# Kernel tuning notes

Hardware: AMD Instinct MI355X
Metric: run time of the kernel (lower is better)

The kernel has to match this reference:

```python
import jax, jax.numpy as jnp
import numpy as np
from jax import lax

WS = 8      # window size (square)
SS = 4      # shift size
HEADS = 8
K = 9       # snake-conv kernel size
CENTER = K // 2
EXT = 1.0   # extend_scope


def _shift_attn_mask(H, W):
    # static numpy construction of Swin shift mask -> [num_windows, L, L]
    m = np.zeros((H, W), dtype=np.float32)
    cnt = 0
    for hs in [(0, -WS), (-WS, -SS), (-SS, None)]:
        for ws_ in [(0, -WS), (-WS, -SS), (-SS, None)]:
            m[hs[0]:hs[1], ws_[0]:ws_[1]] = cnt
            cnt += 1
    m = m.reshape(H // WS, WS, W // WS, WS).transpose(0, 2, 1, 3).reshape(-1, WS * WS)
    d = m[:, None, :] - m[:, :, None]
    return jnp.asarray(np.where(d != 0, -100.0, 0.0).astype(np.float32))


def shifted_window_attention(x, qkv_w, qkv_b, proj_w, proj_b, rel_bias):
    B, H, W, C = x.shape
    d = C // HEADS
    x = jnp.roll(x, shift=(-SS, -SS), axis=(1, 2))
    nH, nW = H // WS, W // WS
    nwin, L = nH * nW, WS * WS
    # window partition -> [B*nwin, L, C]
    xw = x.reshape(B, nH, WS, nW, WS, C).transpose(0, 1, 3, 2, 4, 5).reshape(B * nwin, L, C)
    qkv = (xw @ qkv_w.T + qkv_b).reshape(B * nwin, L, 3, HEADS, d).transpose(2, 0, 3, 1, 4)
    q, k, v = qkv[0] * (d ** -0.5), qkv[1], qkv[2]
    attn = jnp.einsum('nhld,nhmd->nhlm', q, k) + rel_bias[None]
    amask = _shift_attn_mask(H, W)  # [nwin, L, L]
    attn = attn.reshape(B, nwin, HEADS, L, L) + amask[None, :, None]
    attn = jax.nn.softmax(attn.reshape(B * nwin, HEADS, L, L), axis=-1)
    out = jnp.einsum('nhlm,nhmd->nhld', attn, v).transpose(0, 2, 1, 3).reshape(B * nwin, L, C)
    out = out @ proj_w.T + proj_b
    out = out.reshape(B, nH, nW, WS, WS, C).transpose(0, 1, 3, 2, 4, 5).reshape(B, H, W, C)
    return jnp.roll(out, shift=(SS, SS), axis=(1, 2))


def snake_coordinate_map(offset):
    # offset [B, 2K, Wd, Hd], morph=0: cumulative y offsets from the kernel center
    B, _, Wd, Hd = offset.shape
    y_off = offset[:, :K]
    # y_new[center]=0; y_new[center+i]=sum_{j=1..i} y_off[center+j]; mirror below
    up = jnp.cumsum(y_off[:, CENTER + 1:], axis=1)
    down = jnp.cumsum(y_off[:, :CENTER][:, ::-1], axis=1)[:, ::-1]
    y_cum = jnp.concatenate([down, jnp.zeros((B, 1, Wd, Hd), offset.dtype), up], axis=1)
    y_center = jnp.arange(Wd, dtype=offset.dtype)[None, None, :, None]
    y_new = y_center + EXT * y_cum                              # [B,K,Wd,Hd]
    x_spread = jnp.linspace(-CENTER, CENTER, K, dtype=offset.dtype)[None, :, None, None]
    x_center = jnp.arange(Hd, dtype=offset.dtype)[None, None, None, :]
    x_new = jnp.broadcast_to(x_center + x_spread, (B, K, Wd, Hd))
    # rearrange 'b k w h -> b (w k) h'
    y_map = y_new.transpose(0, 2, 1, 3).reshape(B, Wd * K, Hd)
    x_map = x_new.transpose(0, 2, 1, 3).reshape(B, Wd * K, Hd)
    return y_map, x_map


def bilinear_sample(feat, ymap, xmap):
    Hin, Win = feat.shape[-2], feat.shape[-1]
    y = jnp.clip(ymap, 0.0, Hin - 1.0)
    x = jnp.clip(xmap, 0.0, Win - 1.0)
    y0f, x0f = jnp.floor(y), jnp.floor(x)
    wy, wx = y - y0f, x - x0f
    y0 = y0f.astype(jnp.int32); x0 = x0f.astype(jnp.int32)
    y1 = jnp.minimum(y0 + 1, Hin - 1); x1 = jnp.minimum(x0 + 1, Win - 1)
    g = jax.vmap(lambda f, yy, xx: f[:, yy, xx])  # -> [B,C,Ho,Wo]
    v00 = g(feat, y0, x0); v01 = g(feat, y0, x1)
    v10 = g(feat, y1, x0); v11 = g(feat, y1, x1)
    wy = wy[:, None]; wx = wx[:, None]
    return v00 * (1 - wy) * (1 - wx) + v01 * (1 - wy) * wx + v10 * wy * (1 - wx) + v11 * wy * wx


def _forward(x, qkv_weight, qkv_bias, proj_weight, proj_bias, rel_bias, offset, dsc_weight, dsc_bias):
    y = shifted_window_attention(x, qkv_weight, qkv_bias, proj_weight, proj_bias, rel_bias)
    feat = y.transpose(0, 3, 1, 2)                      # NCHW
    ymap, xmap = snake_coordinate_map(offset)
    samp = bilinear_sample(feat, ymap, xmap)            # [B,C,H*K,W]
    out = lax.conv_general_dilated(samp, dsc_weight, window_strides=(K, 1), padding='VALID',
                                   dimension_numbers=('NCHW', 'OIHW', 'NCHW'))
    return jax.nn.relu(out + dsc_bias[None, :, None, None])


def setup_inputs() -> dict:
    key = jax.random.key(0)
    ks = jax.random.split(key, 9)
    B, H, W, C = 8, 64, 64, 256
    return {
        'x': jax.random.normal(ks[0], (B, H, W, C), jnp.float32),
        'qkv_weight': jax.random.normal(ks[1], (3 * C, C), jnp.float32) * 0.05,
        'qkv_bias': jax.random.normal(ks[2], (3 * C,), jnp.float32) * 0.05,
        'proj_weight': jax.random.normal(ks[3], (C, C), jnp.float32) * 0.05,
        'proj_bias': jax.random.normal(ks[4], (C,), jnp.float32) * 0.05,
        'rel_bias': jax.random.normal(ks[5], (HEADS, WS * WS, WS * WS), jnp.float32) * 0.05,
        'offset': jax.random.normal(ks[6], (B, 2 * K, H, W), jnp.float32),
        'dsc_weight': jax.random.normal(ks[7], (C, C, K, 1), jnp.float32) * 0.02,
        'dsc_bias': jax.random.normal(ks[8], (C,), jnp.float32) * 0.02,
    }


def reference(x, qkv_weight, qkv_bias, proj_weight, proj_bias, rel_bias, offset, dsc_weight, dsc_bias):
    return _forward(x, qkv_weight, qkv_bias, proj_weight, proj_bias, rel_bias, offset, dsc_weight, dsc_bias)
```

## Files before the change

kernel.cpp:

```cpp
#include <hip/hip_runtime.h>
#include <math.h>


#define NFLOAT_BUF 8388608

typedef float f32x4 __attribute__((ext_vector_type(4)));
typedef __bf16 bf16x8 __attribute__((ext_vector_type(8)));
typedef _Float16 f16x8 __attribute__((ext_vector_type(8)));

__device__ inline unsigned pack2_bf16(float a, float b) {
    union { float f; unsigned u; } ua, ub;
    ua.f = a; ub.f = b;
    unsigned ra = (ua.u + 0x7FFFu + ((ua.u >> 16) & 1u)) >> 16;
    unsigned rb = (ub.u + 0x7FFFu + ((ub.u >> 16) & 1u)) & 0xFFFF0000u;
    return (ra & 0xFFFFu) | rb;
}
__device__ inline unsigned short pack1_bf16(float a) {
    union { float f; unsigned u; } v;
    v.f = a;
    return (unsigned short)((v.u + 0x7FFFu + ((v.u >> 16) & 1u)) >> 16);
}

__global__ __launch_bounds__(256) void cvt_bf16_kernel(const float* __restrict__ src,
                                                       unsigned short* __restrict__ dst,
                                                       int n8) {
    int t = blockIdx.x * 256 + threadIdx.x;
    if (t >= n8) return;
    const float4* s = (const float4*)(src + (size_t)t * 8);
    float4 a = s[0], b = s[1];
    uint4 o;
    o.x = pack2_bf16(a.x, a.y); o.y = pack2_bf16(a.z, a.w);
    o.z = pack2_bf16(b.x, b.y); o.w = pack2_bf16(b.z, b.w);
    *(uint4*)(dst + (size_t)t * 8) = o;
}

__global__ __launch_bounds__(256) void transpose_w_kernel(const float* __restrict__ w,
                                                          _Float16* __restrict__ wT) {
    int t = blockIdx.x * 256 + threadIdx.x;
    int o = t / 2304;
    int kk = t - o * 2304;
    int k = kk >> 8, i = kk & 255;
    wT[t] = (_Float16)w[(o * 256 + i) * 9 + k];
}

__global__ __launch_bounds__(256) void ymap_kernel(const float* __restrict__ offset,
                                                   float* __restrict__ ymap) {
    int t = blockIdx.x * 256 + threadIdx.x;
    int hd = t & 63;
    int wd = (t >> 6) & 63;
    int b  = t >> 12;
    const float* op = offset + ((size_t)(b * 18) * 64 + wd) * 64 + hd;
    float yo[9];
    #pragma unroll
    for (int k = 0; k < 9; ++k) yo[k] = op[(size_t)k * 4096];
    float cum[9];
    cum[4] = 0.0f;
    float s = 0.0f;
    for (int j = 3; j >= 0; --j) { s += yo[j]; cum[j] = s; }
    s = 0.0f;
    for (int j = 5; j < 9; ++j) { s += yo[j]; cum[j] = s; }
    float wdf = (float)wd;
    float* yp = ymap + ((size_t)(b * 576 + wd * 9)) * 64 + hd;
    #pragma unroll
    for (int k = 0; k < 9; ++k) yp[(size_t)k * 64] = wdf + cum[k];
}

__global__ __launch_bounds__(256) void qkv_mfma_kernel(
    const unsigned short* __restrict__ xb, const unsigned short* __restrict__ wb,
    const float* __restrict__ qkv_b,
    _Float16* __restrict__ qh, _Float16* __restrict__ kh, _Float16* __restrict__ vt) {

    __shared__ __align__(16) char Asb[8192];
    __shared__ __align__(16) char Bsb[32768];
    __shared__ unsigned rowoff[64];

    int nb = blockIdx.x;
    int m0 = blockIdx.y * 64;
    int tid = threadIdx.x;
    int lane = tid & 63, w = tid >> 6;
    int gw = m0 >> 6;

    if (tid < 64) {
        int l = tid;
        int b = gw >> 6, win = gw & 63;
        int rh = ((win >> 3) << 3) + (l >> 3);
        int rw = ((win & 7) << 3) + (l & 7);
        int sh = (rh + 4) & 63, sw = (rw + 4) & 63;
        rowoff[l] = (unsigned)(((b * 64 + sh) * 64 + sw) * 512);
    }

    f32x4 acc[4][4];
    #pragma unroll
    for (int m = 0; m < 4; ++m)
        #pragma unroll
        for (int n = 0; n < 4; ++n) {
            f32x4 z = {0.0f, 0.0f, 0.0f, 0.0f};
            acc[m][n] = z;
        }

    const char* xc = (const char*)xb;
    const char* wc = (const char*)wb;
    int rA = (lane & 15) * 128;
    int u0 = (((lane >> 4)    ) ^ (lane & 7)) << 4;
    int u1 = ((4 + (lane >> 4)) ^ (lane & 7)) << 4;

    __syncthreads();

    for (int c = 0; c < 4; ++c) {
        #pragma unroll
        for (int r = 0; r < 2; ++r) {
            int pos = r * 256 + tid;
            int row = pos >> 3, u = pos & 7;
            const char* src = xc + rowoff[row] + c * 128 + ((u ^ (row & 7)) << 4);
            __builtin_amdgcn_global_load_lds(
                (const __attribute__((address_space(1))) unsigned int*)src,
                (__attribute__((address_space(3))) unsigned int*)(Asb + pos * 16),
                16, 0, 0);
        }
        #pragma unroll
        for (int r = 0; r < 8; ++r) {
            int pos = r * 256 + tid;
            int n = pos >> 3, u = pos & 7;
            const char* src = wc + (size_t)(nb * 256 + n) * 512 + c * 128 + ((u ^ (n & 7)) << 4);
            __builtin_amdgcn_global_load_lds(
                (const __attribute__((address_space(1))) unsigned int*)src,
                (__attribute__((address_space(3))) unsigned int*)(Bsb + pos * 16),
                16, 0, 0);
        }
        __syncthreads();

        bf16x8 av[4][2], bv[4][2];
        #pragma unroll
        for (int m = 0; m < 4; ++m) {
            av[m][0] = *(const bf16x8*)(Asb + m * 2048 + rA + u0);
            av[m][1] = *(const bf16x8*)(Asb + m * 2048 + rA + u1);
        }
        #pragma unroll
        for (int n = 0; n < 4; ++n) {
            bv[n][0] = *(const bf16x8*)(Bsb + w * 8192 + n * 2048 + rA + u0);
            bv[n][1] = *(const bf16x8*)(Bsb + w * 8192 + n * 2048 + rA + u1);
        }
        #pragma unroll
        for (int m = 0; m < 4; ++m)
            #pragma unroll
            for (int n = 0; n < 4; ++n) {
                acc[m][n] = __builtin_amdgcn_mfma_f32_16x16x32_bf16(av[m][0], bv[n][0], acc[m][n], 0, 0, 0);
                acc[m][n] = __builtin_amdgcn_mfma_f32_16x16x32_bf16(av[m][1], bv[n][1], acc[m][n], 0, 0, 0);
            }
        __syncthreads();
    }

    float scale = (nb == 0) ? 0.17677669529663689f : 1.0f;
    #pragma unroll
    for (int nf = 0; nf < 4; ++nf) {
        int o = w * 64 + nf * 16 + (lane & 15);
        float bias = qkv_b[nb * 256 + o];
        int hh = o >> 5, dd = o & 31;
        if (nb < 2) {
            _Float16* dstb = (nb == 0) ? qh : kh;
            _Float16* base = dstb + ((size_t)(gw * 8 + hh) * 64) * 32 + dd;
            #pragma unroll
            for (int mf = 0; mf < 4; ++mf) {
                int l0 = mf * 16 + (lane >> 4) * 4;
                #pragma unroll
                for (int j = 0; j < 4; ++j)
                    base[(size_t)(l0 + j) * 32] = (_Float16)((acc[mf][nf][j] + bias) * scale);
            }
        } else {
            _Float16* base = vt + ((size_t)(gw * 8 + hh) * 32 + dd) * 64;
            #pragma unroll
            for (int mf = 0; mf < 4; ++mf) {
                int l0 = mf * 16 + (lane >> 4) * 4;
                union { _Float16 x[4]; uint2 u; } pk;
                #pragma unroll
                for (int j = 0; j < 4; ++j) pk.x[j] = (_Float16)(acc[mf][nf][j] + bias);
                *(uint2*)(base + l0) = pk.u;
            }
        }
    }
}

__global__ __launch_bounds__(512) void attn_mfma_kernel(
    const _Float16* __restrict__ qh, const _Float16* __restrict__ kh,
    const _Float16* __restrict__ vt, const float* __restrict__ rel_bias,
    unsigned short* __restrict__ attn_ob) {

    __shared__ __align__(16) char Plds[65536];
    int n = blockIdx.x;
    int win = n & 63;
    int wy = win >> 3, wx = win & 7;
    int tid = threadIdx.x, lane = tid & 63, h = tid >> 6;
    int qc = lane & 15, g = lane >> 4;
    char* P = Plds + h * 8192;

    const _Float16* qp = qh + (size_t)(n * 8 + h) * 2048;
    const _Float16* kp = kh + (size_t)(n * 8 + h) * 2048;
    const _Float16* vp = vt + (size_t)(n * 8 + h) * 2048;
    const float* rb = rel_bias + (size_t)h * 4096;

    int rk[16];
    #pragma unroll
    for (int mt = 0; mt < 4; ++mt)
        #pragma unroll
        for (int j = 0; j < 4; ++j) {
            int key = mt * 16 + g * 4 + j;
            int rh = wy * 8 + (key >> 3), rw = wx * 8 + (key & 7);
            rk[mt * 4 + j] = (rh < 56 ? 0 : (rh < 60 ? 1 : 2)) * 3
                           + (rw < 56 ? 0 : (rw < 60 ? 1 : 2));
        }

    f16x8 kf[4];
    #pragma unroll
    for (int mt = 0; mt < 4; ++mt)
        kf[mt] = *(const f16x8*)(kp + (mt * 16 + qc) * 32 + g * 8);

    #pragma unroll
    for (int nt = 0; nt < 4; ++nt) {
        int q = nt * 16 + qc;
        int rqh = wy * 8 + (q >> 3), rqw = wx * 8 + (q & 7);
        int rq = (rqh < 56 ? 0 : (rqh < 60 ? 1 : 2)) * 3
               + (rqw < 56 ? 0 : (rqw < 60 ? 1 : 2));
        f16x8 qf = *(const f16x8*)(qp + q * 32 + g * 8);

        f32x4 s[4];
        #pragma unroll
        for (int mt = 0; mt < 4; ++mt) {
            f32x4 z = {0.0f, 0.0f, 0.0f, 0.0f};
            s[mt] = __builtin_amdgcn_mfma_f32_16x16x32_f16(kf[mt], qf, z, 0, 0, 0);
        }

        float vals[16];
        #pragma unroll
        for (int mt = 0; mt < 4; ++mt) {
            float4 bv4 = *(const float4*)(rb + q * 64 + mt * 16 + g * 4);
            vals[mt * 4 + 0] = s[mt][0] + bv4.x + (rk[mt * 4 + 0] != rq ? -100.0f : 0.0f);
            vals[mt * 4 + 1] = s[mt][1] + bv4.y + (rk[mt * 4 + 1] != rq ? -100.0f : 0.0f);
            vals[mt * 4 + 2] = s[mt][2] + bv4.z + (rk[mt * 4 + 2] != rq ? -100.0f : 0.0f);
            vals[mt * 4 + 3] = s[mt][3] + bv4.w + (rk[mt * 4 + 3] != rq ? -100.0f : 0.0f);
        }

        float mx = vals[0];
        #pragma unroll
        for (int i = 1; i < 16; ++i) mx = fmaxf(mx, vals[i]);
        mx = fmaxf(mx, __shfl_xor(mx, 16));
        mx = fmaxf(mx, __shfl_xor(mx, 32));

        float sum = 0.0f;
        #pragma unroll
        for (int i = 0; i < 16; ++i) { vals[i] = __expf(vals[i] - mx); sum += vals[i]; }
        sum += __shfl_xor(sum, 16);
        sum += __shfl_xor(sum, 32);
        float inv = 1.0f / sum;

        #pragma unroll
        for (int mt = 0; mt < 4; ++mt) {
            union { _Float16 x[4]; uint2 u; } pk4;
            #pragma unroll
            for (int j = 0; j < 4; ++j) pk4.x[j] = (_Float16)(vals[mt * 4 + j] * inv);
            int off = (mt * 32 + g * 8) ^ ((q & 7) << 4);
            *(uint2*)(P + q * 128 + off) = pk4.u;
        }
    }

    f16x8 pa[4][2];
    #pragma unroll
    for (int im = 0; im < 4; ++im)
        #pragma unroll
        for (int ks = 0; ks < 2; ++ks) {
            int row = im * 16 + qc;
            int off = (ks * 64 + g * 16) ^ ((row & 7) << 4);
            pa[im][ks] = *(const f16x8*)(P + row * 128 + off);
        }
    f16x8 bvv[2][2];
    #pragma unroll
    for (int in = 0; in < 2; ++in)
        #pragma unroll
        for (int ks = 0; ks < 2; ++ks)
            bvv[in][ks] = *(const f16x8*)(vp + (in * 16 + qc) * 64 + ks * 32 + g * 8);

    f32x4 acc[4][2];
    #pragma unroll
    for (int im = 0; im < 4; ++im)
        #pragma unroll
        for (int in = 0; in < 2; ++in) {
            f32x4 z = {0.0f, 0.0f, 0.0f, 0.0f};
            acc[im][in] = z;
        }
    #pragma unroll
    for (int im = 0; im < 4; ++im)
        #pragma unroll
        for (int in = 0; in < 2; ++in) {
            acc[im][in] = __builtin_amdgcn_mfma_f32_16x16x32_f16(pa[im][0], bvv[in][0], acc[im][in], 0, 0, 0);
            acc[im][in] = __builtin_amdgcn_mfma_f32_16x16x32_f16(pa[im][1], bvv[in][1], acc[im][in], 0, 0, 0);
        }

    #pragma unroll
    for (int im = 0; im < 4; ++im)
        #pragma unroll
        for (int in = 0; in < 2; ++in)
            #pragma unroll
            for (int j = 0; j < 4; ++j) {
                int q2 = im * 16 + g * 4 + j;
                attn_ob[(size_t)(n * 64 + q2) * 256 + h * 32 + in * 16 + qc] =
                    pack1_bf16(acc[im][in][j]);
            }
}

__global__ __launch_bounds__(256) void proj_mfma_kernel(
    const unsigned short* __restrict__ attn_ob, const unsigned short* __restrict__ pwb,
    const float* __restrict__ proj_b, _Float16* __restrict__ feath) {

    __shared__ __align__(16) char Asb[8192];
    __shared__ __align__(16) char Bsb[32768];

    int m0 = blockIdx.x * 64;
    int tid = threadIdx.x;
    int lane = tid & 63, w = tid >> 6;
    int gw = m0 >> 6;
    int bidx = gw >> 6, win = gw & 63;

    f32x4 acc[4][4];
    #pragma unroll
    for (int m = 0; m < 4; ++m)
        #pragma unroll
        for (int n = 0; n < 4; ++n) {
            f32x4 z = {0.0f, 0.0f, 0.0f, 0.0f};
            acc[m][n] = z;
        }

    const char* ac = (const char*)attn_ob;
    const char* wc = (const char*)pwb;
    int rA = (lane & 15) * 128;
    int u0 = (((lane >> 4)    ) ^ (lane & 7)) << 4;
    int u1 = ((4 + (lane >> 4)) ^ (lane & 7)) << 4;

    for (int c = 0; c < 4; ++c) {
        #pragma unroll
        for (int r = 0; r < 2; ++r) {
            int pos = r * 256 + tid;
            int row = pos >> 3, u = pos & 7;
            const char* src = ac + (size_t)(m0 + row) * 512 + c * 128 + ((u ^ (row & 7)) << 4);
            __builtin_amdgcn_global_load_lds(
                (const __attribute__((address_space(1))) unsigned int*)src,
                (__attribute__((address_space(3))) unsigned int*)(Asb + pos * 16),
                16, 0, 0);
        }
        #pragma unroll
        for (int r = 0; r < 8; ++r) {
            int pos = r * 256 + tid;
            int n = pos >> 3, u = pos & 7;
            const char* src = wc + (size_t)n * 512 + c * 128 + ((u ^ (n & 7)) << 4);
            __builtin_amdgcn_global_load_lds(
                (const __attribute__((address_space(1))) unsigned int*)src,
                (__attribute__((address_space(3))) unsigned int*)(Bsb + pos * 16),
                16, 0, 0);
        }
        __syncthreads();

        bf16x8 av[4][2], bv[4][2];
        #pragma unroll
        for (int m = 0; m < 4; ++m) {
            av[m][0] = *(const bf16x8*)(Asb + m * 2048 + rA + u0);
            av[m][1] = *(const bf16x8*)(Asb + m * 2048 + rA + u1);
        }
        #pragma unroll
        for (int n = 0; n < 4; ++n) {
            bv[n][0] = *(const bf16x8*)(Bsb + w * 8192 + n * 2048 + rA + u0);
            bv[n][1] = *(const bf16x8*)(Bsb + w * 8192 + n * 2048 + rA + u1);
        }
        #pragma unroll
        for (int m = 0; m < 4; ++m)
            #pragma unroll
            for (int n = 0; n < 4; ++n) {
                acc[m][n] = __builtin_amdgcn_mfma_f32_16x16x32_bf16(av[m][0], bv[n][0], acc[m][n], 0, 0, 0);
                acc[m][n] = __builtin_amdgcn_mfma_f32_16x16x32_bf16(av[m][1], bv[n][1], acc[m][n], 0, 0, 0);
            }
        __syncthreads();
    }

    #pragma unroll
    for (int nf = 0; nf < 4; ++nf) {
        int f = w * 64 + nf * 16 + (lane & 15);
        float bias = proj_b[f];
        #pragma unroll
        for (int mf = 0; mf < 4; ++mf) {
            #pragma unroll
            for (int j = 0; j < 4; ++j) {
                int px = mf * 16 + (lane >> 4) * 4 + j;
                int rh = ((win >> 3) << 3) + (px >> 3);
                int rw = ((win & 7) << 3) + (px & 7);
                int p = (rh + 4) & 63;
                int qq = (rw + 4) & 63;
                feath[((size_t)(bidx * 64 + p) * 64 + qq) * 256 + f] =
                    (_Float16)(acc[mf][nf][j] + bias);
            }
        }
    }
}

__global__ __launch_bounds__(512) void sample_conv_mfma4_kernel(
    const _Float16* __restrict__ feath, const float* __restrict__ ymap,
    const _Float16* __restrict__ wT2h, const float* __restrict__ dsc_b,
    float* __restrict__ out) {

    __shared__ __align__(16) char Ab[2][16384];
    __shared__ __align__(16) char Bb[2][32768];
    __shared__ unsigned row0[2][9][64];
    __shared__ unsigned row1[2][9][64];
    __shared__ float    wyv[2][9][64];

    int blk = blockIdx.x;
    int b = blk & 7, wd0 = (blk >> 3) * 2;
    int tid = threadIdx.x;
    int lane = tid & 63, w = tid >> 6;
    int qc = lane & 15, g = lane >> 4;
    int ph = w >> 2, nq = w & 3;

    for (int idx = tid; idx < 1152; idx += 512) {
        int wdl = idx / 576;
        int r = idx - wdl * 576;
        int k = r >> 6, hd = r & 63;
        int wd = wd0 + wdl;
        float y = ymap[((size_t)(b * 576 + wd * 9 + k)) * 64 + hd];
        y = fminf(fmaxf(y, 0.0f), 63.0f);
        float y0f = floorf(y);
        int y0 = (int)y0f;
        int y1 = min(y0 + 1, 63);
        int xc = min(max(hd + k - 4, 0), 63);
        row0[wdl][k][hd] = (unsigned)(((b * 64 + y0) * 64 + xc) * 512);
        row1[wdl][k][hd] = (unsigned)(((b * 64 + y1) * 64 + xc) * 512);
        wyv[wdl][k][hd] = y - y0f;
    }

    f32x4 acc[4][4];
    #pragma unroll
    for (int m = 0; m < 4; ++m)
        #pragma unroll
        for (int n = 0; n < 4; ++n) {
            f32x4 z = {0.0f, 0.0f, 0.0f, 0.0f};
            acc[m][n] = z;
        }

    const char* featc = (const char*)feath;
    const char* wc    = (const char*)wT2h;

    int pxA[2], sAv[2];
    #pragma unroll
    for (int r = 0; r < 2; ++r) {
        int pos = r * 512 + tid;
        pxA[r] = pos >> 3;
        sAv[r] = pos & 7;
    }

    int rAa = qc * 128;
    int u0 = ((g    ) ^ (qc & 7)) << 4;
    int u1 = ((4 + g) ^ (qc & 7)) << 4;

    __syncthreads();

    #pragma unroll
    for (int r = 0; r < 4; ++r) {
        int pos = r * 512 + tid;
        int n = pos >> 3, uu = pos & 7;
        const char* src = wc + n * 4608 + 0 * 128 + ((uu ^ (n & 7)) << 4);
        __builtin_amdgcn_global_load_lds(
            (const __attribute__((address_space(1))) unsigned int*)src,
            (__attribute__((address_space(3))) unsigned int*)(Bb[0] + pos * 16),
            16, 0, 0);
    }
    #pragma unroll
    for (int r = 0; r < 2; ++r) {
        int px = pxA[r], sA = sAv[r];
        int wdl = px >> 6, hd = px & 63;
        unsigned b0 = row0[wdl][0][hd] + sA * 16;
        unsigned b1 = row1[wdl][0][hd] + sA * 16;
        float wy = wyv[wdl][0][hd];
        f16x8 v0 = *(const f16x8*)(featc + b0);
        f16x8 v1 = *(const f16x8*)(featc + b1);
        _Float16 wyh = (_Float16)wy;
        _Float16 omh = (_Float16)(1.0f - wy);
        f16x8 res = v0 * omh + v1 * wyh;
        *(f16x8*)(Ab[0] + px * 128 + ((sA ^ (px & 7)) << 4)) = res;
    }
    __syncthreads();

    for (int c = 0; c < 36; ++c) {
        int cur = c & 1, nxt = cur ^ 1;

        f16x8 s0[2], s1[2];
        float swy[2];
        if (c < 35) {
            int cn = c + 1;
            int ks = cn >> 2, cib = (cn & 3) * 128;
            #pragma unroll
            for (int r = 0; r < 4; ++r) {
                int pos = r * 512 + tid;
                int n = pos >> 3, uu = pos & 7;
                const char* src = wc + n * 4608 + cn * 128 + ((uu ^ (n & 7)) << 4);
                __builtin_amdgcn_global_load_lds(
                    (const __attribute__((address_space(1))) unsigned int*)src,
                    (__attribute__((address_space(3))) unsigned int*)(Bb[nxt] + pos * 16),
                    16, 0, 0);
            }
            #pragma unroll
            for (int r = 0; r < 2; ++r) {
                int px = pxA[r], sA = sAv[r];
                int wdl = px >> 6, hd = px & 63;
                unsigned b0 = row0[wdl][ks][hd] + cib + sA * 16;
                unsigned b1 = row1[wdl][ks][hd] + cib + sA * 16;
                swy[r] = wyv[wdl][ks][hd];
                s0[r] = *(const f16x8*)(featc + b0);
                s1[r] = *(const f16x8*)(featc + b1);
            }
        }

        f16x8 av[4][2], bv[4][2];
        #pragma unroll
        for (int m = 0; m < 4; ++m) {
            char* abase = Ab[cur] + ph * 8192 + m * 2048 + rAa;
            av[m][0] = *(const f16x8*)(abase + u0);
            av[m][1] = *(const f16x8*)(abase + u1);
        }
        #pragma unroll
        for (int n = 0; n < 4; ++n) {
            char* bbase = Bb[cur] + nq * 8192 + n * 2048 + rAa;
            bv[n][0] = *(const f16x8*)(bbase + u0);
            bv[n][1] = *(const f16x8*)(bbase + u1);
        }
        #pragma unroll
        for (int m = 0; m < 4; ++m)
            #pragma unroll
            for (int n = 0; n < 4; ++n) {
                acc[m][n] = __builtin_amdgcn_mfma_f32_16x16x32_f16(av[m][0], bv[n][0], acc[m][n], 0, 0, 0);
                acc[m][n] = __builtin_amdgcn_mfma_f32_16x16x32_f16(av[m][1], bv[n][1], acc[m][n], 0, 0, 0);
            }

        if (c < 35) {
            #pragma unroll
            for (int r = 0; r < 2; ++r) {
                int px = pxA[r], sA = sAv[r];
                _Float16 wyh = (_Float16)swy[r];
                _Float16 omh = (_Float16)(1.0f - swy[r]);
                f16x8 res = s0[r] * omh + s1[r] * wyh;
                *(f16x8*)(Ab[nxt] + px * 128 + ((sA ^ (px & 7)) << 4)) = res;
            }
        }
        __syncthreads();
    }

    #pragma unroll
    for (int n = 0; n < 4; ++n) {
        int o = nq * 64 + n * 16 + qc;
        float bvs = dsc_b[o];
        float* orow = out + ((size_t)(b * 256 + o) * 64 + (wd0 + ph)) * 64;
        #pragma unroll
        for (int m = 0; m < 4; ++m) {
            int px = m * 16 + g * 4;
            float4 res;
            res.x = fmaxf(acc[m][n][0] + bvs, 0.0f);
            res.y = fmaxf(acc[m][n][1] + bvs, 0.0f);
            res.z = fmaxf(acc[m][n][2] + bvs, 0.0f);
            res.w = fmaxf(acc[m][n][3] + bvs, 0.0f);
            *(float4*)(orow + px) = res;
        }
    }
}

extern "C" void kernel_launch(void* const* d_in, const int* in_sizes, int n_in,
                              void* d_out, int out_size, void* d_ws, size_t ws_size,
                              hipStream_t stream) {
    (void)in_sizes; (void)n_in; (void)out_size; (void)ws_size;
    const float* x        = (const float*)d_in[0];
    const float* qkv_w    = (const float*)d_in[1];
    const float* qkv_b    = (const float*)d_in[2];
    const float* proj_w   = (const float*)d_in[3];
    const float* proj_b   = (const float*)d_in[4];
    const float* rel_bias = (const float*)d_in[5];
    const float* offset   = (const float*)d_in[6];
    const float* dsc_w    = (const float*)d_in[7];
    const float* dsc_b    = (const float*)d_in[8];
    float* out = (float*)d_out;

    unsigned short* wsu = (unsigned short*)d_ws;
    _Float16* qh = (_Float16*)wsu;
    _Float16* kh = (_Float16*)(wsu + NFLOAT_BUF);
    _Float16* vt = (_Float16*)(wsu + 2 * (size_t)NFLOAT_BUF);
    unsigned short* attn_ob = wsu + 3 * (size_t)NFLOAT_BUF;
    _Float16* feath = (_Float16*)(wsu + 4 * (size_t)NFLOAT_BUF);
    unsigned short* xb      = wsu + 5 * (size_t)NFLOAT_BUF;
    unsigned short* wb      = wsu + 6 * (size_t)NFLOAT_BUF;
    unsigned short* pwb     = wb + 196608;
    _Float16* wT2h          = (_Float16*)(pwb + 65536);
    float* ymap = (float*)((unsigned short*)wT2h + 589824);

    cvt_bf16_kernel<<<4096, 256, 0, stream>>>(x, xb, 1048576);
    cvt_bf16_kernel<<<96, 256, 0, stream>>>(qkv_w, wb, 24576);
    cvt_bf16_kernel<<<32, 256, 0, stream>>>(proj_w, pwb, 8192);
    transpose_w_kernel<<<2304, 256, 0, stream>>>(dsc_w, wT2h);
    ymap_kernel<<<128, 256, 0, stream>>>(offset, ymap);
    qkv_mfma_kernel<<<dim3(3, 512), 256, 0, stream>>>(xb, wb, qkv_b, qh, kh, vt);
    attn_mfma_kernel<<<512, 512, 0, stream>>>(qh, kh, vt, rel_bias, attn_ob);
    proj_mfma_kernel<<<512, 256, 0, stream>>>(attn_ob, pwb, proj_b, feath);
    sample_conv_mfma4_kernel<<<256, 512, 0, stream>>>(feath, ymap, wT2h, dsc_b, out);
}
```

Baseline: 222.4 us.

## Fuse prep kernels into one launch and fuse output projection into attention

Five small preprocessing kernels are merged into one launch that dispatches work by block index. The attention kernel now keeps each window's attention output in LDS as fp16 and runs the output projection in place, so the attn_ob round trip through global memory and a separate kernel launch are no longer needed. The projection weights switch from bf16 to fp16, and the attention kernel gains a launch-bounds occupancy hint. In exchange, the fused kernel reuses its 64KB of LDS, which needs extra barriers, and it reloads the projection weights for every window block.

```diff
diff --git a/kernel.cpp b/kernel.cpp
--- a/kernel.cpp
+++ b/kernel.cpp
@@ -15,54 +15,70 @@
     unsigned rb = (ub.u + 0x7FFFu + ((ub.u >> 16) & 1u)) & 0xFFFF0000u;
     return (ra & 0xFFFFu) | rb;
 }
-__device__ inline unsigned short pack1_bf16(float a) {
-    union { float f; unsigned u; } v;
-    v.f = a;
-    return (unsigned short)((v.u + 0x7FFFu + ((v.u >> 16) & 1u)) >> 16);
-}
-
-__global__ __launch_bounds__(256) void cvt_bf16_kernel(const float* __restrict__ src,
-                                                       unsigned short* __restrict__ dst,
-                                                       int n8) {
-    int t = blockIdx.x * 256 + threadIdx.x;
-    if (t >= n8) return;
-    const float4* s = (const float4*)(src + (size_t)t * 8);
-    float4 a = s[0], b = s[1];
-    uint4 o;
-    o.x = pack2_bf16(a.x, a.y); o.y = pack2_bf16(a.z, a.w);
-    o.z = pack2_bf16(b.x, b.y); o.w = pack2_bf16(b.z, b.w);
-    *(uint4*)(dst + (size_t)t * 8) = o;
-}
-
-__global__ __launch_bounds__(256) void transpose_w_kernel(const float* __restrict__ w,
-                                                          _Float16* __restrict__ wT) {
-    int t = blockIdx.x * 256 + threadIdx.x;
-    int o = t / 2304;
-    int kk = t - o * 2304;
-    int k = kk >> 8, i = kk & 255;
-    wT[t] = (_Float16)w[(o * 256 + i) * 9 + k];
-}
-
-__global__ __launch_bounds__(256) void ymap_kernel(const float* __restrict__ offset,
-                                                   float* __restrict__ ymap) {
-    int t = blockIdx.x * 256 + threadIdx.x;
-    int hd = t & 63;
-    int wd = (t >> 6) & 63;
-    int b  = t >> 12;
-    const float* op = offset + ((size_t)(b * 18) * 64 + wd) * 64 + hd;
-    float yo[9];
-    #pragma unroll
-    for (int k = 0; k < 9; ++k) yo[k] = op[(size_t)k * 4096];
-    float cum[9];
-    cum[4] = 0.0f;
-    float s = 0.0f;
-    for (int j = 3; j >= 0; --j) { s += yo[j]; cum[j] = s; }
-    s = 0.0f;
-    for (int j = 5; j < 9; ++j) { s += yo[j]; cum[j] = s; }
-    float wdf = (float)wd;
-    float* yp = ymap + ((size_t)(b * 576 + wd * 9)) * 64 + hd;
-    #pragma unroll
-    for (int k = 0; k < 9; ++k) yp[(size_t)k * 64] = wdf + cum[k];
+
+__global__ __launch_bounds__(256) void prep_kernel(
+    const float* __restrict__ x, unsigned short* __restrict__ xb,
+    const float* __restrict__ qkv_w, unsigned short* __restrict__ wb,
+    const float* __restrict__ proj_w, _Float16* __restrict__ pwh,
+    const float* __restrict__ dsc_w, _Float16* __restrict__ wT,
+    const float* __restrict__ offset, float* __restrict__ ymap) {
+    int bid = blockIdx.x, tid = threadIdx.x;
+    if (bid < 4096) {
+        int t = bid * 256 + tid;
+        const float4* s = (const float4*)(x + (size_t)t * 8);
+        float4 a = s[0], b = s[1];
+        uint4 o;
+        o.x = pack2_bf16(a.x, a.y); o.y = pack2_bf16(a.z, a.w);
+        o.z = pack2_bf16(b.x, b.y); o.w = pack2_bf16(b.z, b.w);
+        *(uint4*)(xb + (size_t)t * 8) = o;
+    } else if (bid < 4192) {
+        int t = (bid - 4096) * 256 + tid;
+        if (t < 24576) {
+            const float4* s = (const float4*)(qkv_w + (size_t)t * 8);
+            float4 a = s[0], b = s[1];
+            uint4 o;
+            o.x = pack2_bf16(a.x, a.y); o.y = pack2_bf16(a.z, a.w);
+            o.z = pack2_bf16(b.x, b.y); o.w = pack2_bf16(b.z, b.w);
+            *(uint4*)(wb + (size_t)t * 8) = o;
+        }
+    } else if (bid < 4224) {
+        int t = (bid - 4192) * 256 + tid;
+        if (t < 8192) {
+            const float4* s = (const float4*)(proj_w + (size_t)t * 8);
+            float4 a = s[0], b = s[1];
+            union { _Float16 h[8]; uint4 u; } o;
+            o.h[0] = (_Float16)a.x; o.h[1] = (_Float16)a.y;
+            o.h[2] = (_Float16)a.z; o.h[3] = (_Float16)a.w;
+            o.h[4] = (_Float16)b.x; o.h[5] = (_Float16)b.y;
+            o.h[6] = (_Float16)b.z; o.h[7] = (_Float16)b.w;
+            *(uint4*)(pwh + (size_t)t * 8) = o.u;
+        }
+    } else if (bid < 6528) {
+        int t = (bid - 4224) * 256 + tid;
+        int o = t / 2304;
+        int kk = t - o * 2304;
+        int k = kk >> 8, i = kk & 255;
+        wT[t] = (_Float16)dsc_w[(o * 256 + i) * 9 + k];
+    } else {
+        int t = (bid - 6528) * 256 + tid;
+        int hd = t & 63;
+        int wd = (t >> 6) & 63;
+        int b  = t >> 12;
+        const float* op = offset + ((size_t)(b * 18) * 64 + wd) * 64 + hd;
+        float yo[9];
+        #pragma unroll
+        for (int k = 0; k < 9; ++k) yo[k] = op[(size_t)k * 4096];
+        float cum[9];
+        cum[4] = 0.0f;
+        float s = 0.0f;
+        for (int j = 3; j >= 0; --j) { s += yo[j]; cum[j] = s; }
+        s = 0.0f;
+        for (int j = 5; j < 9; ++j) { s += yo[j]; cum[j] = s; }
+        float wdf = (float)wd;
+        float* yp = ymap + ((size_t)(b * 576 + wd * 9)) * 64 + hd;
+        #pragma unroll
+        for (int k = 0; k < 9; ++k) yp[(size_t)k * 64] = wdf + cum[k];
+    }
 }
 
 __global__ __launch_bounds__(256) void qkv_mfma_kernel(
@@ -180,18 +196,19 @@
     }
 }
 
-__global__ __launch_bounds__(512) void attn_mfma_kernel(
+__global__ __launch_bounds__(512, 4) void attn_proj_kernel(
     const _Float16* __restrict__ qh, const _Float16* __restrict__ kh,
     const _Float16* __restrict__ vt, const float* __restrict__ rel_bias,
-    unsigned short* __restrict__ attn_ob) {
-
-    __shared__ __align__(16) char Plds[65536];
+    const _Float16* __restrict__ pwh, const float* __restrict__ proj_b,
+    _Float16* __restrict__ feath) {
+
+    __shared__ __align__(16) char SH[65536];
     int n = blockIdx.x;
     int win = n & 63;
     int wy = win >> 3, wx = win & 7;
     int tid = threadIdx.x, lane = tid & 63, h = tid >> 6;
     int qc = lane & 15, g = lane >> 4;
-    char* P = Plds + h * 8192;
+    char* P = SH + h * 8192;
 
     const _Float16* qp = qh + (size_t)(n * 8 + h) * 2048;
     const _Float16* kp = kh + (size_t)(n * 8 + h) * 2048;
@@ -294,62 +311,42 @@
             acc[im][in] = __builtin_amdgcn_mfma_f32_16x16x32_f16(pa[im][1], bvv[in][1], acc[im][in], 0, 0, 0);
         }
 
+    __syncthreads();
+
+    char* aob = SH;
+    char* Bsb = SH + 32768;
     #pragma unroll
     for (int im = 0; im < 4; ++im)
         #pragma unroll
         for (int in = 0; in < 2; ++in)
             #pragma unroll
             for (int j = 0; j < 4; ++j) {
-                int q2 = im * 16 + g * 4 + j;
-                attn_ob[(size_t)(n * 64 + q2) * 256 + h * 32 + in * 16 + qc] =
-                    pack1_bf16(acc[im][in][j]);
-            }
-}
-
-__global__ __launch_bounds__(256) void proj_mfma_kernel(
-    const unsigned short* __restrict__ attn_ob, const unsigned short* __restrict__ pwb,
-    const float* __restrict__ proj_b, _Float16* __restrict__ feath) {
-
-    __shared__ __align__(16) char Asb[8192];
-    __shared__ __align__(16) char Bsb[32768];
-
-    int m0 = blockIdx.x * 64;
-    int tid = threadIdx.x;
-    int lane = tid & 63, w = tid >> 6;
-    int gw = m0 >> 6;
-    int bidx = gw >> 6, win = gw & 63;
-
-    f32x4 acc[4][4];
-    #pragma unroll
-    for (int m = 0; m < 4; ++m)
-        #pragma unroll
-        for (int n = 0; n < 4; ++n) {
+                int row = im * 16 + g * 4 + j;
+                int f = h * 32 + in * 16 + qc;
+                *(_Float16*)(aob + row * 512 + ((((f >> 3) ^ (row & 7)) << 4) + (f & 7) * 2)) =
+                    (_Float16)acc[im][in][j];
+            }
+    __syncthreads();
+
+    int w04 = h & 3, wm = h >> 2;
+    const char* wcp = (const char*)pwh;
+    int bidx = n >> 6;
+
+    f32x4 pacc[2][4];
+    #pragma unroll
+    for (int m = 0; m < 2; ++m)
+        #pragma unroll
+        for (int nn = 0; nn < 4; ++nn) {
             f32x4 z = {0.0f, 0.0f, 0.0f, 0.0f};
-            acc[m][n] = z;
-        }
-
-    const char* ac = (const char*)attn_ob;
-    const char* wc = (const char*)pwb;
-    int rA = (lane & 15) * 128;
-    int u0 = (((lane >> 4)    ) ^ (lane & 7)) << 4;
-    int u1 = ((4 + (lane >> 4)) ^ (lane & 7)) << 4;
+            pacc[m][nn] = z;
+        }
 
     for (int c = 0; c < 4; ++c) {
         #pragma unroll
-        for (int r = 0; r < 2; ++r) {
-            int pos = r * 256 + tid;
-            int row = pos >> 3, u = pos & 7;
-            const char* src = ac + (size_t)(m0 + row) * 512 + c * 128 + ((u ^ (row & 7)) << 4);
-            __builtin_amdgcn_global_load_lds(
-                (const __attribute__((address_space(1))) unsigned int*)src,
-                (__attribute__((address_space(3))) unsigned int*)(Asb + pos * 16),
-                16, 0, 0);
-        }
-        #pragma unroll
-        for (int r = 0; r < 8; ++r) {
-            int pos = r * 256 + tid;
-            int n = pos >> 3, u = pos & 7;
-            const char* src = wc + (size_t)n * 512 + c * 128 + ((u ^ (n & 7)) << 4);
+        for (int r = 0; r < 4; ++r) {
+            int pos = r * 512 + tid;
+            int nr = pos >> 3, uu = pos & 7;
+            const char* src = wcp + (size_t)nr * 512 + c * 128 + ((uu ^ (nr & 7)) << 4);
             __builtin_amdgcn_global_load_lds(
                 (const __attribute__((address_space(1))) unsigned int*)src,
                 (__attribute__((address_space(3))) unsigned int*)(Bsb + pos * 16),
@@ -357,42 +354,48 @@
         }
         __syncthreads();
 
-        bf16x8 av[4][2], bv[4][2];
-        #pragma unroll
-        for (int m = 0; m < 4; ++m) {
-            av[m][0] = *(const bf16x8*)(Asb + m * 2048 + rA + u0);
-            av[m][1] = *(const bf16x8*)(Asb + m * 2048 + rA + u1);
-        }
-        #pragma unroll
-        for (int n = 0; n < 4; ++n) {
-            bv[n][0] = *(const bf16x8*)(Bsb + w * 8192 + n * 2048 + rA + u0);
-            bv[n][1] = *(const bf16x8*)(Bsb + w * 8192 + n * 2048 + rA + u1);
-        }
-        #pragma unroll
-        for (int m = 0; m < 4; ++m)
-            #pragma unroll
-            for (int n = 0; n < 4; ++n) {
-                acc[m][n] = __builtin_amdgcn_mfma_f32_16x16x32_bf16(av[m][0], bv[n][0], acc[m][n], 0, 0, 0);
-                acc[m][n] = __builtin_amdgcn_mfma_f32_16x16x32_bf16(av[m][1], bv[n][1], acc[m][n], 0, 0, 0);
+        f16x8 av2[2][2], bv2[4][2];
+        #pragma unroll
+        for (int m = 0; m < 2; ++m) {
+            int row = wm * 32 + m * 16 + qc;
+            #pragma unroll
+            for (int ks = 0; ks < 2; ++ks) {
+                int u = c * 8 + ks * 4 + g;
+                av2[m][ks] = *(const f16x8*)(aob + row * 512 + ((u ^ (row & 7)) << 4));
+            }
+        }
+        #pragma unroll
+        for (int nn = 0; nn < 4; ++nn) {
+            int oc = w04 * 64 + nn * 16 + qc;
+            #pragma unroll
+            for (int ks = 0; ks < 2; ++ks)
+                bv2[nn][ks] = *(const f16x8*)(Bsb + oc * 128 + (((ks * 4 + g) ^ (oc & 7)) << 4));
+        }
+        #pragma unroll
+        for (int m = 0; m < 2; ++m)
+            #pragma unroll
+            for (int nn = 0; nn < 4; ++nn) {
+                pacc[m][nn] = __builtin_amdgcn_mfma_f32_16x16x32_f16(av2[m][0], bv2[nn][0], pacc[m][nn], 0, 0, 0);
+                pacc[m][nn] = __builtin_amdgcn_mfma_f32_16x16x32_f16(av2[m][1], bv2[nn][1], pacc[m][nn], 0, 0, 0);
             }
         __syncthreads();
     }
 
     #pragma unroll
-    for (int nf = 0; nf < 4; ++nf) {
-        int f = w * 64 + nf * 16 + (lane & 15);
+    for (int nn = 0; nn < 4; ++nn) {
+        int f = w04 * 64 + nn * 16 + qc;
         float bias = proj_b[f];
         #pragma unroll
-        for (int mf = 0; mf < 4; ++mf) {
+        for (int m = 0; m < 2; ++m) {
             #pragma unroll
             for (int j = 0; j < 4; ++j) {
-                int px = mf * 16 + (lane >> 4) * 4 + j;
+                int px = wm * 32 + m * 16 + g * 4 + j;
                 int rh = ((win >> 3) << 3) + (px >> 3);
                 int rw = ((win & 7) << 3) + (px & 7);
                 int p = (rh + 4) & 63;
                 int qq = (rw + 4) & 63;
                 feath[((size_t)(bidx * 64 + p) * 64 + qq) * 256 + f] =
-                    (_Float16)(acc[mf][nf][j] + bias);
+                    (_Float16)(pacc[m][nn][j] + bias);
             }
         }
     }
@@ -585,21 +588,16 @@
     _Float16* qh = (_Float16*)wsu;
     _Float16* kh = (_Float16*)(wsu + NFLOAT_BUF);
     _Float16* vt = (_Float16*)(wsu + 2 * (size_t)NFLOAT_BUF);
-    unsigned short* attn_ob = wsu + 3 * (size_t)NFLOAT_BUF;
-    _Float16* feath = (_Float16*)(wsu + 4 * (size_t)NFLOAT_BUF);
-    unsigned short* xb      = wsu + 5 * (size_t)NFLOAT_BUF;
-    unsigned short* wb      = wsu + 6 * (size_t)NFLOAT_BUF;
-    unsigned short* pwb     = wb + 196608;
-    _Float16* wT2h          = (_Float16*)(pwb + 65536);
+    _Float16* feath = (_Float16*)(wsu + 3 * (size_t)NFLOAT_BUF);
+    unsigned short* xb      = wsu + 4 * (size_t)NFLOAT_BUF;
+    unsigned short* wb      = wsu + 5 * (size_t)NFLOAT_BUF;
+    _Float16* pwh           = (_Float16*)(wb + 196608);
+    _Float16* wT2h          = (_Float16*)((unsigned short*)pwh + 65536);
     float* ymap = (float*)((unsigned short*)wT2h + 589824);
 
-    cvt_bf16_kernel<<<4096, 256, 0, stream>>>(x, xb, 1048576);
-    cvt_bf16_kernel<<<96, 256, 0, stream>>>(qkv_w, wb, 24576);
-    cvt_bf16_kernel<<<32, 256, 0, stream>>>(proj_w, pwb, 8192);
-    transpose_w_kernel<<<2304, 256, 0, stream>>>(dsc_w, wT2h);
-    ymap_kernel<<<128, 256, 0, stream>>>(offset, ymap);
+    prep_kernel<<<6656, 256, 0, stream>>>(x, xb, qkv_w, wb, proj_w, pwh,
+                                          dsc_w, wT2h, offset, ymap);
     qkv_mfma_kernel<<<dim3(3, 512), 256, 0, stream>>>(xb, wb, qkv_b, qh, kh, vt);
-    attn_mfma_kernel<<<512, 512, 0, stream>>>(qh, kh, vt, rel_bias, attn_ob);
-    proj_mfma_kernel<<<512, 256, 0, stream>>>(attn_ob, pwb, proj_b, feath);
+    attn_proj_kernel<<<512, 512, 0, stream>>>(qh, kh, vt, rel_bias, pwh, proj_b, feath);
     sample_conv_mfma4_kernel<<<256, 512, 0, stream>>>(feath, ymap, wT2h, dsc_b, out);
 }
```

Result: faster. 204.7 us (-8.0%).
